# Optimization experiments

Measured on AMD Instinct MI355X. Metric: run time of the kernel, lower is better.

## Reference

```python
import jax, jax.numpy as jnp
import numpy as np

DIM = 1024
NUM_HEADS = 16
HEAD_DIM = DIM // NUM_HEADS
SEQ = 2048
BATCH = 2


def setup_inputs() -> dict:
    key = jax.random.key(0)
    kx, kq, kk, kv, ko, kb = jax.random.split(key, 6)
    s = 0.02
    return {
        "x": jax.random.normal(kx, (BATCH, SEQ, DIM), dtype=jnp.float32),
        "W_q": jax.random.normal(kq, (DIM, DIM), dtype=jnp.float32) * s,
        "W_k": jax.random.normal(kk, (DIM, DIM), dtype=jnp.float32) * s,
        "W_v": jax.random.normal(kv, (DIM, DIM), dtype=jnp.float32) * s,
        "W_o": jax.random.normal(ko, (DIM, DIM), dtype=jnp.float32) * s,
        "b_o": jax.random.normal(kb, (DIM,), dtype=jnp.float32) * s,
    }


def reference(x, W_q, W_k, W_v, W_o, b_o):
    b, n, d = x.shape
    # Linear layers (torch Linear: y = x @ W.T); weights here stored as [out, in]
    q = jnp.einsum('bnd,ed->bne', x, W_q).reshape(b, n, NUM_HEADS, HEAD_DIM)
    k = jnp.einsum('bnd,ed->bne', x, W_k).reshape(b, n, NUM_HEADS, HEAD_DIM)
    v = jnp.einsum('bnd,ed->bne', x, W_v).reshape(b, n, NUM_HEADS, HEAD_DIM)
    # scores: [b, h, q, k]
    scores = jnp.einsum('bqhd,bkhd->bhqk', q, k)
    causal = jnp.tril(jnp.ones((n, n), dtype=bool))  # True = keep
    scores = jnp.where(causal, scores, -jnp.inf)
    weights = jax.nn.softmax(scores / jnp.sqrt(jnp.float32(HEAD_DIM)), axis=-1)
    ctx = jnp.einsum('bhqk,bkhd->bqhd', weights, v).reshape(b, n, d)
    return jnp.einsum('bnd,ed->bne', ctx, W_o) + b_o
```

## Files before the change

### kernel.cpp

```cpp
#include <hip/hip_runtime.h>
#include <hip/hip_bf16.h>

#define DIM 1024
#define NHEADS 16
#define HD 64
#define SEQ 2048
#define BATCH 2
#define MROWS (BATCH * SEQ)
#define MB (1024u * 1024u)
#define NT (SEQ / 64)

typedef __bf16 bf16x8 __attribute__((ext_vector_type(8)));
typedef float f32x4 __attribute__((ext_vector_type(4)));
typedef short short8 __attribute__((ext_vector_type(8)));

#define SCQ (0.125f * 1.44269504f)

__device__ __forceinline__ unsigned short f2bf(float f) {
    union { float f; unsigned u; } v; v.f = f;
    unsigned r = v.u + 0x7fffu + ((v.u >> 16) & 1u);
    return (unsigned short)(r >> 16);
}
__device__ __forceinline__ unsigned cvtpk(float lo, float hi) {
    unsigned r;
    asm("v_cvt_pk_bf16_f32 %0, %1, %2" : "=v"(r) : "v"(lo), "v"(hi));
    return r;
}

__device__ __forceinline__ void gld16(const unsigned short* g, unsigned short* l) {
    __builtin_amdgcn_global_load_lds(
        (const __attribute__((address_space(1))) void*)g,
        (__attribute__((address_space(3))) void*)l, 16, 0, 0);
}

#define VWAIT(n) asm volatile("s_waitcnt vmcnt(" #n ")" ::: "memory")
#define BARRIER  do { __builtin_amdgcn_s_barrier(); __builtin_amdgcn_sched_barrier(0); } while (0)

__global__ __launch_bounds__(256) void f2all_kernel(
    const float* __restrict__ x,
    const float* __restrict__ w0, const float* __restrict__ w1,
    const float* __restrict__ w2, const float* __restrict__ w3,
    unsigned short* __restrict__ xb,
    unsigned short* __restrict__ o0, unsigned short* __restrict__ o1,
    unsigned short* __restrict__ o2, unsigned short* __restrict__ o3)
{
    const float* in; unsigned short* out; int n4;
    switch (blockIdx.y) {
        case 0: in = x;  out = xb; n4 = (MROWS * DIM) / 4; break;
        case 1: in = w0; out = o0; n4 = (DIM * DIM) / 4;   break;
        case 2: in = w1; out = o1; n4 = (DIM * DIM) / 4;   break;
        case 3: in = w2; out = o2; n4 = (DIM * DIM) / 4;   break;
        default: in = w3; out = o3; n4 = (DIM * DIM) / 4;  break;
    }
    for (int i = blockIdx.x * 256 + threadIdx.x; i < n4; i += 1024 * 256) {
        float4 v = ((const float4*)in)[i];
        ushort4 o;
        o.x = f2bf(v.x); o.y = f2bf(v.y); o.z = f2bf(v.z); o.w = f2bf(v.w);
        ((ushort4*)out)[i] = o;
    }
}


#define GEMM_VARS(Aptr, Bptr)                                                  \
    __shared__ unsigned short As[3][128 * 32];                                 \
    __shared__ unsigned short Bs[3][128 * 32];                                 \
    const int tid  = threadIdx.x;                                              \
    const int lane = tid & 63;                                                 \
    const int wid  = tid >> 6;                                                 \
    const int wrow = wid >> 1, wcol = wid & 1;                                 \
    const int l15  = lane & 15;                                                \
    const int lhi  = lane >> 4;                                                \
    f32x4 acc[4][4] = {};                                                      \
    const int r0s = tid >> 2;                                                  \
    const int c0s = (tid & 3) ^ ((r0s >> 1) & 3);                              \
    const int r1s = (tid + 256) >> 2;                                          \
    const int c1s = (tid & 3) ^ ((r1s >> 1) & 3);                              \
    const unsigned short* gA0 = (Aptr) + (size_t)(row0 + r0s) * DIM + c0s * 8; \
    const unsigned short* gA1 = (Aptr) + (size_t)(row0 + r1s) * DIM + c1s * 8; \
    const unsigned short* gB0 = (Bptr) + (size_t)(col0 + r0s) * DIM + c0s * 8; \
    const unsigned short* gB1 = (Bptr) + (size_t)(col0 + r1s) * DIM + c1s * 8;

#define GEMM_STAGE(bi, kofs)                                                   \
    gld16(gA0 + (kofs), &As[bi][tid * 8]);                                     \
    gld16(gA1 + (kofs), &As[bi][(tid + 256) * 8]);                             \
    gld16(gB0 + (kofs), &Bs[bi][tid * 8]);                                     \
    gld16(gB1 + (kofs), &Bs[bi][(tid + 256) * 8]);

#define GEMM_COMPUTE(bi)                                                       \
    {   const unsigned short* Ac = &As[bi][0];                                 \
        const unsigned short* Bc = &Bs[bi][0];                                 \
        bf16x8 af[4], bfr[4];                                                  \
        _Pragma("unroll")                                                      \
        for (int m = 0; m < 4; m++) {                                          \
            int r = wrow * 64 + m * 16 + l15;                                  \
            int c = lhi ^ ((r >> 1) & 3);                                      \
            af[m] = *(const bf16x8*)&Ac[r * 32 + c * 8];                       \
        }                                                                      \
        _Pragma("unroll")                                                      \
        for (int n = 0; n < 4; n++) {                                          \
            int r = wcol * 64 + n * 16 + l15;                                  \
            int c = lhi ^ ((r >> 1) & 3);                                      \
            bfr[n] = *(const bf16x8*)&Bc[r * 32 + c * 8];                      \
        }                                                                      \
        __builtin_amdgcn_s_setprio(1);                                         \
        _Pragma("unroll")                                                      \
        for (int m = 0; m < 4; m++)                                            \
            _Pragma("unroll")                                                  \
            for (int n = 0; n < 4; n++)                                        \
                acc[m][n] = __builtin_amdgcn_mfma_f32_16x16x32_bf16(           \
                    af[m], bfr[n], acc[m][n], 0, 0, 0);                        \
        __builtin_amdgcn_s_setprio(0);                                         \
    }

#define GEMM_PIPELINE()                                                        \
    GEMM_STAGE(0, 0)                                                           \
    GEMM_STAGE(1, 32)                                                          \
    int bi = 0;                                                                \
    for (int k0 = 0; k0 + 96 <= DIM; k0 += 32) {                               \
        VWAIT(4);                                                              \
        BARRIER;                                                               \
        int b2 = bi + 2; if (b2 >= 3) b2 -= 3;                                 \
        GEMM_STAGE(b2, k0 + 64)                                                \
        GEMM_COMPUTE(bi)                                                       \
        bi = (bi + 1 == 3) ? 0 : bi + 1;                                       \
    }                                                                          \
    VWAIT(4);                                                                  \
    BARRIER;                                                                   \
    GEMM_COMPUTE(bi)                                                           \
    bi = (bi + 1 == 3) ? 0 : bi + 1;                                           \
    VWAIT(0);                                                                  \
    BARRIER;                                                                   \
    GEMM_COMPUTE(bi)

__global__ __launch_bounds__(256) void qkv_gemm(
    const unsigned short* __restrict__ A,
    const unsigned short* __restrict__ Wqb,
    const unsigned short* __restrict__ Wkb,
    const unsigned short* __restrict__ Wvb,
    unsigned short* __restrict__ Qb,
    unsigned short* __restrict__ Kbf,
    unsigned short* __restrict__ Vtb)
{
    const int lb  = ((int)blockIdx.x & 7) * 96 + ((int)blockIdx.x >> 3);
    const int xx  = lb % 24;
    const int yy  = lb / 24;
    const int sel = xx >> 3;
    const unsigned short* Bw = (sel == 0) ? Wqb : ((sel == 1) ? Wkb : Wvb);
    const int row0 = yy * 128;
    const int col0 = (xx & 7) * 128;

    GEMM_VARS(A, Bw)
    GEMM_PIPELINE()

    const int cr = lhi * 4;
    unsigned short* outRM = (sel == 0) ? Qb : Kbf;
    #pragma unroll
    for (int m = 0; m < 4; m++) {
        #pragma unroll
        for (int n = 0; n < 4; n++) {
            int gc = col0 + wcol * 64 + n * 16 + l15;
            if (sel < 2) {
                #pragma unroll
                for (int j2 = 0; j2 < 4; j2++) {
                    int gr = row0 + wrow * 64 + m * 16 + cr + j2;
                    float v = acc[m][n][j2];
                    if (sel == 0) v *= SCQ;
                    outRM[(size_t)gr * DIM + gc] = f2bf(v);
                }
            } else {
                int gr0 = row0 + wrow * 64 + m * 16 + cr;
                int bb = gr0 >> 11, s0 = gr0 & 2047;
                int hh = gc >> 6,  d = gc & 63;
                ushort4 pv4;
                pv4.x = f2bf(acc[m][n][0]);
                pv4.y = f2bf(acc[m][n][1]);
                pv4.z = f2bf(acc[m][n][2]);
                pv4.w = f2bf(acc[m][n][3]);
                *(ushort4*)&Vtb[(((size_t)bb * NHEADS + hh) * HD + d) * SEQ + s0] = pv4;
            }
        }
    }
}

__global__ __launch_bounds__(256) void o_gemm(
    const unsigned short* __restrict__ A,
    const unsigned short* __restrict__ Bw,
    float* __restrict__ Cp,
    const float* __restrict__ bias)
{
    __shared__ unsigned short As[3][64 * 32];
    __shared__ unsigned short Bs[3][64 * 32];

    const int lb  = ((int)blockIdx.x & 7) * 128 + ((int)blockIdx.x >> 3);
    const int xx  = lb % 16;
    const int yy  = lb / 16;
    const int row0 = yy * 64;
    const int col0 = xx * 64;

    const int tid  = threadIdx.x;
    const int lane = tid & 63;
    const int wid  = tid >> 6;
    const int wrow = wid >> 1, wcol = wid & 1;
    const int l15  = lane & 15;
    const int lhi  = lane >> 4;
    f32x4 acc[2][2] = {};

    const int r0s = tid >> 2;
    const int c0s = (tid & 3) ^ ((r0s >> 1) & 3);
    const unsigned short* gA0 = A  + (size_t)(row0 + r0s) * DIM + c0s * 8;
    const unsigned short* gB0 = Bw + (size_t)(col0 + r0s) * DIM + c0s * 8;

#define OSTAGE(bi, kofs)                                     \
    gld16(gA0 + (kofs), &As[bi][tid * 8]);                   \
    gld16(gB0 + (kofs), &Bs[bi][tid * 8]);

#define OCOMPUTE(bi)                                                           \
    {   const unsigned short* Ac = &As[bi][0];                                 \
        const unsigned short* Bc = &Bs[bi][0];                                 \
        bf16x8 af[2], bfr[2];                                                  \
        _Pragma("unroll")                                                      \
        for (int m = 0; m < 2; m++) {                                          \
            int r = wrow * 32 + m * 16 + l15;                                  \
            int c = lhi ^ ((r >> 1) & 3);                                      \
            af[m] = *(const bf16x8*)&Ac[r * 32 + c * 8];                       \
        }                                                                      \
        _Pragma("unroll")                                                      \
        for (int n = 0; n < 2; n++) {                                          \
            int r = wcol * 32 + n * 16 + l15;                                  \
            int c = lhi ^ ((r >> 1) & 3);                                      \
            bfr[n] = *(const bf16x8*)&Bc[r * 32 + c * 8];                      \
        }                                                                      \
        __builtin_amdgcn_s_setprio(1);                                         \
        _Pragma("unroll")                                                      \
        for (int m = 0; m < 2; m++)                                            \
            _Pragma("unroll")                                                  \
            for (int n = 0; n < 2; n++)                                        \
                acc[m][n] = __builtin_amdgcn_mfma_f32_16x16x32_bf16(           \
                    af[m], bfr[n], acc[m][n], 0, 0, 0);                        \
        __builtin_amdgcn_s_setprio(0);                                         \
    }

    OSTAGE(0, 0)
    OSTAGE(1, 32)
    int bi = 0;
    for (int k0 = 0; k0 + 96 <= DIM; k0 += 32) {
        VWAIT(2);
        BARRIER;
        int b2 = bi + 2; if (b2 >= 3) b2 -= 3;
        OSTAGE(b2, k0 + 64)
        OCOMPUTE(bi)
        bi = (bi + 1 == 3) ? 0 : bi + 1;
    }
    VWAIT(2);
    BARRIER;
    OCOMPUTE(bi)
    bi = (bi + 1 == 3) ? 0 : bi + 1;
    VWAIT(0);
    BARRIER;
    OCOMPUTE(bi)
#undef OSTAGE
#undef OCOMPUTE

    const int cr = lhi * 4;
    #pragma unroll
    for (int m = 0; m < 2; m++) {
        #pragma unroll
        for (int n = 0; n < 2; n++) {
            #pragma unroll
            for (int j = 0; j < 4; j++) {
                int gr = row0 + wrow * 32 + m * 16 + cr + j;
                int gc = col0 + wcol * 32 + n * 16 + l15;
                Cp[(size_t)gr * DIM + gc] = acc[m][n][j] + bias[gc];
            }
        }
    }
}

#define ATTN_CORE(bi, t, MASKED)                                               \
    {   const unsigned short* Kc = &Ks[bi][0];                                 \
        const unsigned short* Vc = &Vs[bi][0];                                 \
        f32x4 sacc[4] = {};                                                    \
        __builtin_amdgcn_s_setprio(1);                                         \
        _Pragma("unroll")                                                      \
        for (int ks = 0; ks < 2; ++ks) {                                       \
            bf16x8 bq = ks ? aq1 : aq0;                                        \
            _Pragma("unroll")                                                  \
            for (int nt = 0; nt < 4; nt++) {                                   \
                int r = nt * 16 + l15;                                         \
                int c = (ks * 4 + lhi) ^ (r & 7);                              \
                bf16x8 ak = *(const bf16x8*)&Kc[r * 64 + c * 8];               \
                sacc[nt] = __builtin_amdgcn_mfma_f32_16x16x32_bf16(            \
                    ak, bq, sacc[nt], 0, 0, 0);                                \
            }                                                                  \
        }                                                                      \
        __builtin_amdgcn_s_setprio(0);                                         \
        _Pragma("unroll")                                                      \
        for (int nt = 0; nt < 4; nt++) {                                       \
            float pv[4];                                                       \
            _Pragma("unroll")                                                  \
            for (int j = 0; j < 4; j++) {                                      \
                if (MASKED && (nt * 16 + lhi * 4 + j > (w & 3) * 16 + l15))    \
                    pv[j] = 0.f;                                               \
                else                                                           \
                    pv[j] = exp2f(sacc[nt][j]);                                \
            }                                                                  \
            *(uint2*)&Ps[w][l15][nt * 16 + lhi * 4] =                          \
                make_uint2(cvtpk(pv[0], pv[1]), cvtpk(pv[2], pv[3]));          \
        }                                                                      \
              \
        bf16x8 bv[2][4];                                                       \
        _Pragma("unroll")                                                      \
        for (int ks = 0; ks < 2; ++ks)                                         \
            _Pragma("unroll")                                                  \
            for (int dt = 0; dt < 4; dt++) {                                   \
                int r = dt * 16 + l15;                                         \
                int c = (ks * 4 + lhi) ^ (r & 7);                              \
                bv[ks][dt] = *(const bf16x8*)&Vc[r * 64 + c * 8];              \
            }                                                                  \
        _Pragma("unroll")                                                      \
        for (int ks = 0; ks < 2; ++ks) {                                       \
            bf16x8 ap = *(const bf16x8*)&Ps[w][l15][ks * 32 + lhi * 8];        \
            __builtin_amdgcn_s_setprio(1);                                     \
            _Pragma("unroll")                                                  \
            for (int dt = 0; dt < 4; dt++)                                     \
                octx[dt] = __builtin_amdgcn_mfma_f32_16x16x32_bf16(            \
                    ap, bv[ks][dt], octx[dt], 0, 0, 0);                        \
            octxS = __builtin_amdgcn_mfma_f32_16x16x32_bf16(ap, vones, octxS, 0, 0, 0); \
            __builtin_amdgcn_s_setprio(0);                                     \
        }                                                                      \
    }

__global__ __launch_bounds__(512) void attn_kernel(
    const unsigned short* __restrict__ Q,
    const unsigned short* __restrict__ Kb,
    const unsigned short* __restrict__ Vt,
    unsigned short* __restrict__ Ctx)
{
    __shared__ unsigned short Ks[2][64 * 64];
    __shared__ unsigned short Vs[2][64 * 64];
    __shared__ unsigned short Ps[8][16][72];

    const int tid  = threadIdx.x;
    const int lane = tid & 63;
    const int w    = tid >> 6;
    const int bid  = (int)blockIdx.x;
    const int half = bid >> 8;
    const int idx  = bid & 255;
    const int h    = idx & 15;
    const int b    = (idx >> 4) & 1;
    const int slot = idx >> 5;
    const int p    = half ? slot : (15 - slot);
    const int l15  = lane & 15;
    const int lhi  = lane >> 4;

    const int qblk   = 2 * p + (w >> 2);
    const int qw     = qblk * 64 + (w & 3) * 16;
    const int ntiles = 2 * p + 2;

    const size_t qrow = ((size_t)b * SEQ + qw + l15) * DIM + h * HD;
    bf16x8 aq0 = *(const bf16x8*)(Q + qrow + lhi * 8);
    bf16x8 aq1 = *(const bf16x8*)(Q + qrow + 32 + lhi * 8);

    const int srow = tid >> 3;
    const int sc16 = (tid & 7) ^ (srow & 7);
    const unsigned short* gK = Kb + ((size_t)b * SEQ + srow) * DIM + h * HD + sc16 * 8;
    const unsigned short* gV = Vt + (((size_t)b * NHEADS + h) * HD + srow) * SEQ + sc16 * 8;

    bf16x8 vones;
    #pragma unroll
    for (int i = 0; i < 8; i++) vones[i] = (__bf16)1.0f;

    f32x4 octx[4] = {};
    f32x4 octxS = {};

    gld16(gK, &Ks[0][tid * 8]);
    gld16(gV, &Vs[0][tid * 8]);
    VWAIT(0);
    BARRIER;

    int cur = 0;
    for (int t = 0; t < ntiles; ++t) {
        if (t + 1 < ntiles) {
            gld16(gK + (size_t)(t + 1) * 64 * DIM, &Ks[cur ^ 1][tid * 8]);
            gld16(gV + (size_t)(t + 1) * 64,       &Vs[cur ^ 1][tid * 8]);
        }
        if (t < qblk) {
            ATTN_CORE(cur, t, false)
        } else if (t == qblk) {
            ATTN_CORE(cur, t, true)
        }
        VWAIT(0);
        BARRIER;
        cur ^= 1;
    }

    #pragma unroll
    for (int j = 0; j < 4; j++) {
        float inv = 1.0f / octxS[j];
        #pragma unroll
        for (int dt = 0; dt < 4; dt++) {
            Ctx[((size_t)b * SEQ + qw + lhi * 4 + j) * DIM + h * HD + dt * 16 + l15] =
                f2bf(octx[dt][j] * inv);
        }
    }
}

extern "C" void kernel_launch(void* const* d_in, const int* in_sizes, int n_in,
                              void* d_out, int out_size, void* d_ws, size_t ws_size,
                              hipStream_t stream) {
    const float* x  = (const float*)d_in[0];
    const float* Wq = (const float*)d_in[1];
    const float* Wk = (const float*)d_in[2];
    const float* Wv = (const float*)d_in[3];
    const float* Wo = (const float*)d_in[4];
    const float* bo = (const float*)d_in[5];

    char* ws = (char*)d_ws;
    unsigned short* xb   = (unsigned short*)(ws + 0 * MB);
    unsigned short* Wqb  = (unsigned short*)(ws + 8 * MB);
    unsigned short* Wkb  = (unsigned short*)(ws + 10 * MB);
    unsigned short* Wvb  = (unsigned short*)(ws + 12 * MB);
    unsigned short* Wob  = (unsigned short*)(ws + 14 * MB);
    unsigned short* Qb   = (unsigned short*)(ws + 16 * MB);
    unsigned short* Kbf  = (unsigned short*)(ws + 24 * MB);
    unsigned short* Vtb  = (unsigned short*)(ws + 32 * MB);
    unsigned short* ctxb = (unsigned short*)(ws + 40 * MB);

    f2all_kernel<<<dim3(1024, 5), 256, 0, stream>>>(x, Wq, Wk, Wv, Wo,
                                                    xb, Wqb, Wkb, Wvb, Wob);

    qkv_gemm<<<768, 256, 0, stream>>>(xb, Wqb, Wkb, Wvb, Qb, Kbf, Vtb);

    attn_kernel<<<512, 512, 0, stream>>>(Qb, Kbf, Vtb, ctxb);

    o_gemm<<<1024, 256, 0, stream>>>(ctxb, Wob, (float*)d_out, bo);
}
```

Measured before the change: 108.5 us.

## Split KV range of heavy causal query blocks across two workgroups with combine pass

The attention grid grows from 512 to 768 workgroups. Each of the longer causal query blocks (p >= 8) is split into two workgroups that each process half of the KV tiles. Each half writes unnormalized bf16 partial context and fp32 row sums to workspace, and a new combine kernel adds the halves and normalizes. Short query blocks still write their context directly. This cuts the longest per-workgroup tile chain to even out load across CUs, at the cost of an extra launch, about 8MB of partial-result traffic, and an extra bf16 rounding of the partials.

Result: slower. 118.0 us (+8.7%).

```diff
diff --git a/kernel.cpp b/kernel.cpp
--- a/kernel.cpp
+++ b/kernel.cpp
@@ -20,6 +20,10 @@
     union { float f; unsigned u; } v; v.f = f;
     unsigned r = v.u + 0x7fffu + ((v.u >> 16) & 1u);
     return (unsigned short)(r >> 16);
+}
+__device__ __forceinline__ float bf2f(unsigned short h) {
+    union { unsigned u; float f; } v; v.u = ((unsigned)h) << 16;
+    return v.f;
 }
 __device__ __forceinline__ unsigned cvtpk(float lo, float hi) {
     unsigned r;
@@ -59,7 +63,6 @@
         ((ushort4*)out)[i] = o;
     }
 }
-
 
 #define GEMM_VARS(Aptr, Bptr)                                                  \
     __shared__ unsigned short As[3][128 * 32];                                 \
@@ -307,7 +310,6 @@
             *(uint2*)&Ps[w][l15][nt * 16 + lhi * 4] =                          \
                 make_uint2(cvtpk(pv[0], pv[1]), cvtpk(pv[2], pv[3]));          \
         }                                                                      \
-              \
         bf16x8 bv[2][4];                                                       \
         _Pragma("unroll")                                                      \
         for (int ks = 0; ks < 2; ++ks)                                         \
@@ -334,7 +336,9 @@
     const unsigned short* __restrict__ Q,
     const unsigned short* __restrict__ Kb,
     const unsigned short* __restrict__ Vt,
-    unsigned short* __restrict__ Ctx)
+    unsigned short* __restrict__ Ctx,
+    unsigned short* __restrict__ pb,
+    float* __restrict__ sb)
 {
     __shared__ unsigned short Ks[2][64 * 64];
     __shared__ unsigned short Vs[2][64 * 64];
@@ -344,18 +348,22 @@
     const int lane = tid & 63;
     const int w    = tid >> 6;
     const int bid  = (int)blockIdx.x;
-    const int half = bid >> 8;
-    const int idx  = bid & 255;
-    const int h    = idx & 15;
-    const int b    = (idx >> 4) & 1;
-    const int slot = idx >> 5;
-    const int p    = half ? slot : (15 - slot);
+    const bool heavy = (bid < 512);
+    int half, p, h, b;
+    if (heavy) {
+        int hp = bid >> 1; half = bid & 1;
+        h = hp & 15; b = (hp >> 4) & 1; p = 15 - (hp >> 5);
+    } else {
+        int idx = bid - 512; half = 0;
+        h = idx & 15; b = (idx >> 4) & 1; p = 7 - (idx >> 5);
+    }
+    const int lo = (heavy && half) ? (p + 1) : 0;
+    const int hi = (heavy && !half) ? (p + 1) : (2 * p + 2);
     const int l15  = lane & 15;
     const int lhi  = lane >> 4;
 
-    const int qblk   = 2 * p + (w >> 2);
-    const int qw     = qblk * 64 + (w & 3) * 16;
-    const int ntiles = 2 * p + 2;
+    const int qblk = 2 * p + (w >> 2);
+    const int qw   = qblk * 64 + (w & 3) * 16;
 
     const size_t qrow = ((size_t)b * SEQ + qw + l15) * DIM + h * HD;
     bf16x8 aq0 = *(const bf16x8*)(Q + qrow + lhi * 8);
@@ -373,14 +381,14 @@
     f32x4 octx[4] = {};
     f32x4 octxS = {};
 
-    gld16(gK, &Ks[0][tid * 8]);
-    gld16(gV, &Vs[0][tid * 8]);
+    gld16(gK + (size_t)lo * 64 * DIM, &Ks[0][tid * 8]);
+    gld16(gV + (size_t)lo * 64,       &Vs[0][tid * 8]);
     VWAIT(0);
     BARRIER;
 
     int cur = 0;
-    for (int t = 0; t < ntiles; ++t) {
-        if (t + 1 < ntiles) {
+    for (int t = lo; t < hi; ++t) {
+        if (t + 1 < hi) {
             gld16(gK + (size_t)(t + 1) * 64 * DIM, &Ks[cur ^ 1][tid * 8]);
             gld16(gV + (size_t)(t + 1) * 64,       &Vs[cur ^ 1][tid * 8]);
         }
@@ -394,14 +402,57 @@
         cur ^= 1;
     }
 
+    if (heavy) {
+        #pragma unroll
+        for (int j = 0; j < 4; j++) {
+            int lr = (w >> 2) * 64 + (w & 3) * 16 + lhi * 4 + j;
+            size_t rbase = ((((size_t)half * 2 + b) * 16 + h) * 8 + (p - 8)) * 128 + lr;
+            #pragma unroll
+            for (int dt = 0; dt < 4; dt++)
+                pb[rbase * 64 + dt * 16 + l15] = f2bf(octx[dt][j]);
+            if (l15 == 0) sb[rbase] = octxS[j];
+        }
+    } else {
+        #pragma unroll
+        for (int j = 0; j < 4; j++) {
+            float inv = 1.0f / octxS[j];
+            #pragma unroll
+            for (int dt = 0; dt < 4; dt++) {
+                Ctx[((size_t)b * SEQ + qw + lhi * 4 + j) * DIM + h * HD + dt * 16 + l15] =
+                    f2bf(octx[dt][j] * inv);
+            }
+        }
+    }
+}
+
+__global__ __launch_bounds__(256) void combine_kernel(
+    const unsigned short* __restrict__ pb,
+    const float* __restrict__ sb,
+    unsigned short* __restrict__ Ctx)
+{
+    int row = blockIdx.x * 256 + threadIdx.x;
+    int lr   = row & 127;
+    int pidx = (row >> 7) & 7;
+    int h    = (row >> 10) & 15;
+    int b    = row >> 14;
+    float inv = 1.0f / (sb[row] + sb[row + 32768]);
+    int q = (pidx + 8) * 128 + lr;
+    const unsigned short* pA = pb + (size_t)row * 64;
+    const unsigned short* pB = pA + (size_t)32768 * 64;
+    unsigned short* out = Ctx + ((size_t)b * SEQ + q) * DIM + h * HD;
     #pragma unroll
-    for (int j = 0; j < 4; j++) {
-        float inv = 1.0f / octxS[j];
-        #pragma unroll
-        for (int dt = 0; dt < 4; dt++) {
-            Ctx[((size_t)b * SEQ + qw + lhi * 4 + j) * DIM + h * HD + dt * 16 + l15] =
-                f2bf(octx[dt][j] * inv);
-        }
+    for (int c = 0; c < 64; c += 8) {
+        ushort4 o0, o1;
+        o0.x = f2bf((bf2f(pA[c + 0]) + bf2f(pB[c + 0])) * inv);
+        o0.y = f2bf((bf2f(pA[c + 1]) + bf2f(pB[c + 1])) * inv);
+        o0.z = f2bf((bf2f(pA[c + 2]) + bf2f(pB[c + 2])) * inv);
+        o0.w = f2bf((bf2f(pA[c + 3]) + bf2f(pB[c + 3])) * inv);
+        o1.x = f2bf((bf2f(pA[c + 4]) + bf2f(pB[c + 4])) * inv);
+        o1.y = f2bf((bf2f(pA[c + 5]) + bf2f(pB[c + 5])) * inv);
+        o1.z = f2bf((bf2f(pA[c + 6]) + bf2f(pB[c + 6])) * inv);
+        o1.w = f2bf((bf2f(pA[c + 7]) + bf2f(pB[c + 7])) * inv);
+        *(ushort4*)(out + c)     = o0;
+        *(ushort4*)(out + c + 4) = o1;
     }
 }
 
@@ -425,13 +476,17 @@
     unsigned short* Kbf  = (unsigned short*)(ws + 24 * MB);
     unsigned short* Vtb  = (unsigned short*)(ws + 32 * MB);
     unsigned short* ctxb = (unsigned short*)(ws + 40 * MB);
+    unsigned short* pb   = (unsigned short*)(ws + 0 * MB);
+    float*          sbuf = (float*)(ws + 8 * MB);
 
     f2all_kernel<<<dim3(1024, 5), 256, 0, stream>>>(x, Wq, Wk, Wv, Wo,
                                                     xb, Wqb, Wkb, Wvb, Wob);
 
     qkv_gemm<<<768, 256, 0, stream>>>(xb, Wqb, Wkb, Wvb, Qb, Kbf, Vtb);
 
-    attn_kernel<<<512, 512, 0, stream>>>(Qb, Kbf, Vtb, ctxb);
+    attn_kernel<<<768, 512, 0, stream>>>(Qb, Kbf, Vtb, ctxb, pb, sbuf);
+
+    combine_kernel<<<128, 256, 0, stream>>>(pb, sbuf, ctxb);
 
     o_gemm<<<1024, 256, 0, stream>>>(ctxb, Wob, (float*)d_out, bo);
 }
```
